# Performance work log

Hardware: AMD Instinct MI355X
Metric: run time of the kernel (lower is better)

The kernel has to match this reference:

```python
import jax, jax.numpy as jnp
import numpy as np

D_MODEL = 1024
HEAD = 16
D_K = D_MODEL // HEAD
NEG_INF = -1.0e9


def setup_inputs() -> dict:
    key = jax.random.key(0)
    ks = jax.random.split(key, 12)
    B, S = 2, 2048
    scale = 1.0 / np.sqrt(D_MODEL)
    inp = {
        "query": jax.random.normal(ks[0], (B, S, D_MODEL), jnp.float32),
        "key": jax.random.normal(ks[1], (B, S, D_MODEL), jnp.float32),
        "value": jax.random.normal(ks[2], (B, S, D_MODEL), jnp.float32),
        "mask": jax.random.randint(ks[3], (B, 1, 1, S), 0, 2, jnp.int32),
        "Wq": jax.random.normal(ks[4], (D_MODEL, D_MODEL), jnp.float32) * scale,
        "bq": jnp.zeros((D_MODEL,), jnp.float32),
        "Wk": jax.random.normal(ks[5], (D_MODEL, D_MODEL), jnp.float32) * scale,
        "bk": jnp.zeros((D_MODEL,), jnp.float32),
        "Wv": jax.random.normal(ks[6], (D_MODEL, D_MODEL), jnp.float32) * scale,
        "bv": jnp.zeros((D_MODEL,), jnp.float32),
        "Wo": jax.random.normal(ks[7], (D_MODEL, D_MODEL), jnp.float32) * scale,
        "bo": jnp.zeros((D_MODEL,), jnp.float32),
    }
    return inp


def reference(query, key, value, mask, Wq, bq, Wk, bk, Wv, bv, Wo, bo):
    B, S, _ = query.shape
    # QKV projections (torch nn.Linear: x @ W^T + b)
    q = query @ Wq.T + bq
    k = key @ Wk.T + bk
    v = value @ Wv.T + bv
    # [B, H, S, d_k]
    q = q.reshape(B, S, HEAD, D_K).transpose(0, 2, 1, 3)
    k = k.reshape(B, S, HEAD, D_K).transpose(0, 2, 1, 3)
    v = v.reshape(B, S, HEAD, D_K).transpose(0, 2, 1, 3)
    # scores [B, H, S, S]
    scores = jnp.einsum("bhqd,bhkd->bhqk", q, k) / jnp.sqrt(jnp.float32(D_K))
    scores = jnp.where(mask == 0, jnp.float32(NEG_INF), scores)
    attn = jax.nn.softmax(scores, axis=-1)  # dropout off (eval mode)
    ctx = jnp.einsum("bhqk,bhkd->bhqd", attn, v)
    ctx = ctx.transpose(0, 2, 1, 3).reshape(B, S, D_MODEL)
    return ctx @ Wo.T + bo
```

## Files before the change

kernel.cpp:

```cpp
#include <hip/hip_runtime.h>
#include <cstdint>
#include <cstddef>

typedef unsigned short u16;
typedef unsigned int   u32;
typedef __bf16 bf16x8 __attribute__((ext_vector_type(8)));
typedef float  f32x4  __attribute__((ext_vector_type(4)));

#define D_MODEL 1024
#define SEQ     2048
#define NTOK    4096
#define NHEAD   16
#define DK      64

__device__ __forceinline__ float fast_exp2(float x) {
  return __builtin_amdgcn_exp2f(x);
}

__device__ __forceinline__ u16 f2bf(float f) {
  u32 u = __builtin_bit_cast(u32, f);
  u += 0x7fffu + ((u >> 16) & 1u);
  return (u16)(u >> 16);
}

__device__ __forceinline__ void gload16(const u16* g, u16* l) {
  __builtin_amdgcn_global_load_lds(
      (__attribute__((address_space(1))) void*)(uintptr_t)g,
      (__attribute__((address_space(3))) void*)l,
      16, 0, 0);
}

__global__ __launch_bounds__(256) void mha_convert(
    const float* __restrict__ q, const float* __restrict__ k,
    const float* __restrict__ v, const float* __restrict__ wq,
    const float* __restrict__ wk, const float* __restrict__ wv,
    const float* __restrict__ wo, u16* __restrict__ xb, u16* __restrict__ wb) {
  const int total = 1 << 22;
  for (int cid = blockIdx.x * blockDim.x + threadIdx.x; cid < total;
       cid += gridDim.x * blockDim.x) {
    const float* src;
    u16* dst;
    int off;
    if (cid < (3 << 20)) {
      int which = cid >> 20;
      off = cid & ((1 << 20) - 1);
      src = which == 0 ? q : (which == 1 ? k : v);
      dst = xb + ((size_t)which << 22);
    } else {
      int cc = cid - (3 << 20);
      int which = cc >> 18;
      off = cc & ((1 << 18) - 1);
      src = which == 0 ? wq : (which == 1 ? wk : (which == 2 ? wv : wo));
      dst = wb + ((size_t)which << 20);
    }
    float4 f = ((const float4*)src)[off];
    ushort4 u;
    u.x = f2bf(f.x); u.y = f2bf(f.y); u.z = f2bf(f.z); u.w = f2bf(f.w);
    ((ushort4*)dst)[off] = u;
  }
}

__global__ __launch_bounds__(256) void gemm_qkv(
    const u16* __restrict__ A, const u16* __restrict__ Bw,
    const float* __restrict__ b0, const float* __restrict__ b1,
    const float* __restrict__ b2, u16* __restrict__ Cout) {
  __shared__ __align__(16) u16 smem[128 * 136];
  u16* sA = smem;
  u16* sB = smem + 128 * 32;

  const int t = threadIdx.x;
  const int z = blockIdx.z;
  const u16* Ap = A + ((size_t)z << 22);
  const u16* Bp = Bw + ((size_t)z << 20);
  const float* bias = (z == 0) ? b0 : ((z == 1) ? b1 : b2);
  const float scl = (z == 0) ? 0.18033688011f : 1.0f;

  const int m0 = blockIdx.y * 128, n0 = blockIdx.x * 128;
  const int lane = t & 63, wv = t >> 6;
  const int wm = (wv >> 1) * 64, wn = (wv & 1) * 64;
  const int c = lane & 15, qd = lane >> 4;

  const int arow = t >> 2, aoff = (t & 3) * 8;
  const u16* ga0 = Ap + (size_t)(m0 + arow) * D_MODEL + aoff;
  const u16* ga1 = Ap + (size_t)(m0 + arow + 64) * D_MODEL + aoff;
  const u16* gb0 = Bp + (size_t)(n0 + arow) * D_MODEL + aoff;
  const u16* gb1 = Bp + (size_t)(n0 + arow + 64) * D_MODEL + aoff;
  u16* la0 = sA + t * 8;
  u16* la1 = sA + (t + 256) * 8;
  u16* lb0 = sB + t * 8;
  u16* lb1 = sB + (t + 256) * 8;

  f32x4 acc[4][4] = {};

  for (int kb = 0; kb < D_MODEL; kb += 32) {
    gload16(ga0 + kb, la0);
    gload16(ga1 + kb, la1);
    gload16(gb0 + kb, lb0);
    gload16(gb1 + kb, lb1);
    __syncthreads();
    bf16x8 af[4], bfr[4];
#pragma unroll
    for (int i = 0; i < 4; ++i)
      af[i] = *(const bf16x8*)&sA[(wm + i * 16 + c) * 32 + qd * 8];
#pragma unroll
    for (int j = 0; j < 4; ++j)
      bfr[j] = *(const bf16x8*)&sB[(wn + j * 16 + c) * 32 + qd * 8];
#pragma unroll
    for (int i = 0; i < 4; ++i)
#pragma unroll
      for (int j = 0; j < 4; ++j)
        acc[i][j] =
            __builtin_amdgcn_mfma_f32_16x16x32_bf16(af[i], bfr[j], acc[i][j], 0, 0, 0);
    __syncthreads();
  }

  u16* sC = smem;
  if (z == 2) {
#pragma unroll
    for (int j = 0; j < 4; ++j) {
      const int col = wn + j * 16 + c;
      const float bv = bias[n0 + col];
#pragma unroll
      for (int i = 0; i < 4; ++i)
#pragma unroll
        for (int r = 0; r < 4; ++r)
          sC[col * 136 + wm + i * 16 + qd * 4 + r] = f2bf(acc[i][j][r] + bv);
    }
    __syncthreads();
    u16* VT = Cout + ((size_t)2 << 22);
    const int bb = m0 >> 11, s0 = m0 & 2047;
    const int sidx = (t & 15) * 8;
#pragma unroll
    for (int outer = 0; outer < 8; ++outer) {
      const int vrow = outer * 16 + (t >> 4);
      const int col = n0 + vrow;
      const int hh = col >> 6, dd = col & 63;
      uint4 val = *(const uint4*)&sC[vrow * 136 + sidx];
      *(uint4*)&VT[((size_t)((bb * NHEAD + hh) * DK + dd)) * SEQ + s0 + sidx] =
          val;
    }
  } else {
#pragma unroll
    for (int j = 0; j < 4; ++j) {
      const int col = wn + j * 16 + c;
      const float bv = bias[n0 + col];
#pragma unroll
      for (int i = 0; i < 4; ++i)
#pragma unroll
        for (int r = 0; r < 4; ++r)
          sC[(wm + i * 16 + qd * 4 + r) * 136 + col] =
              f2bf((acc[i][j][r] + bv) * scl);
    }
    __syncthreads();
    u16* outp = Cout + ((size_t)z << 22);
    const int cidx = (t & 15) * 8;
#pragma unroll
    for (int outer = 0; outer < 8; ++outer) {
      const int lrow = outer * 16 + (t >> 4);
      uint4 val = *(const uint4*)&sC[lrow * 136 + cidx];
      *(uint4*)&outp[(size_t)(m0 + lrow) * D_MODEL + n0 + cidx] = val;
    }
  }
}

__global__ __launch_bounds__(256) void mha_attn(
    const u16* __restrict__ QKVb, const int* __restrict__ mask,
    u16* __restrict__ Opart, float* __restrict__ ml) {
  __shared__ __align__(16) u16 sK[64 * 72];
  __shared__ __align__(16) u16 sVt[64 * 72];
  __shared__ __align__(16) u16 sP[128 * 72];
  __shared__ __align__(16) float sMadd[64];

  const int t = threadIdx.x, lane = t & 63, wq = t >> 6;
  const int c = lane & 15, qd = lane >> 4;
  const int qb = blockIdx.x, h = blockIdx.y;
  const int b = blockIdx.z & 1, ck = blockIdx.z >> 1;

  const u16* Qg = QKVb;
  const u16* Kg = QKVb + ((size_t)4 << 20);
  const u16* VTh = QKVb + ((size_t)8 << 20) +
                   ((size_t)((b * NHEAD + h) * DK)) * SEQ;
  const int rowbase = b * SEQ;
  const int colbase = h * DK;

  bf16x8 aq[2][2];
#pragma unroll
  for (int qt = 0; qt < 2; ++qt) {
    const u16* g = Qg +
                   (size_t)(rowbase + qb * 128 + wq * 32 + qt * 16 + c) * D_MODEL +
                   colbase + qd * 8;
    aq[qt][0] = *(const bf16x8*)g;
    aq[qt][1] = *(const bf16x8*)(g + 32);
  }

  float l[2] = {0.f, 0.f};
  f32x4 o[2][4] = {};
  const float MADD = -1.4426950e9f;
  const float MFIX = 16.0f;

  const int r0s = t >> 2, offs = (t & 3) * 16;
  const u16* gkb = Kg + (size_t)(rowbase + r0s) * D_MODEL + colbase + offs;
  const u16* gvb = VTh + (size_t)r0s * SEQ + offs;

  uint4 k0, k1, v0, v1;
  int mval;
  {
    const int kb = ck * 16;
    const u16* gk = gkb + (size_t)kb * 64 * D_MODEL;
    const u16* gv = gvb + kb * 64;
    k0 = *(const uint4*)gk;
    k1 = *(const uint4*)(gk + 8);
    v0 = *(const uint4*)gv;
    v1 = *(const uint4*)(gv + 8);
    mval = (t < 64) ? mask[b * SEQ + kb * 64 + t] : 1;
  }

  for (int kbi = 0; kbi < 16; ++kbi) {
    __syncthreads();
    *(uint4*)&sK[r0s * 72 + offs] = k0;
    *(uint4*)&sK[r0s * 72 + offs + 8] = k1;
    *(uint4*)&sVt[r0s * 72 + offs] = v0;
    *(uint4*)&sVt[r0s * 72 + offs + 8] = v1;
    if (t < 64) sMadd[t] = (mval == 0) ? MADD : 0.0f;
    __syncthreads();
    if (kbi < 15) {
      const int kb = ck * 16 + kbi + 1;
      const u16* gk = gkb + (size_t)kb * 64 * D_MODEL;
      const u16* gv = gvb + kb * 64;
      k0 = *(const uint4*)gk;
      k1 = *(const uint4*)(gk + 8);
      v0 = *(const uint4*)gv;
      v1 = *(const uint4*)(gv + 8);
      mval = (t < 64) ? mask[b * SEQ + kb * 64 + t] : 1;
    }

    f32x4 st[2][4];
#pragma unroll
    for (int tt = 0; tt < 4; ++tt) {
      bf16x8 ak0 = *(const bf16x8*)&sK[(tt * 16 + c) * 72 + qd * 8];
      bf16x8 ak1 = *(const bf16x8*)&sK[(tt * 16 + c) * 72 + qd * 8 + 32];
      f32x4 cin = *(const f32x4*)&sMadd[tt * 16 + qd * 4];
#pragma unroll
      for (int qt = 0; qt < 2; ++qt) {
        f32x4 a =
            __builtin_amdgcn_mfma_f32_16x16x32_bf16(ak0, aq[qt][0], cin, 0, 0, 0);
        a = __builtin_amdgcn_mfma_f32_16x16x32_bf16(ak1, aq[qt][1], a, 0, 0, 0);
        st[qt][tt] = a;
      }
    }

#pragma unroll
    for (int qt = 0; qt < 2; ++qt) {
      float sum = 0.f;
      const int prow = (wq * 32 + qt * 16 + c) * 72;
#pragma unroll
      for (int tt = 0; tt < 4; ++tt) {
        u32 pk[2];
#pragma unroll
        for (int pr = 0; pr < 2; ++pr) {
          u32 p0 = __builtin_bit_cast(u32, fast_exp2(st[qt][tt][2 * pr] - MFIX));
          u32 p1 =
              __builtin_bit_cast(u32, fast_exp2(st[qt][tt][2 * pr + 1] - MFIX));
          u32 hi1 = p1 & 0xffff0000u;
          pk[pr] = (p0 >> 16) | hi1;
          sum += __builtin_bit_cast(float, p0 & 0xffff0000u);
          sum += __builtin_bit_cast(float, hi1);
        }
        uint2 pv2 = {pk[0], pk[1]};
        *(uint2*)&sP[prow + tt * 16 + qd * 4] = pv2;
      }
      l[qt] += sum;
    }

    bf16x8 bp[2][2];
#pragma unroll
    for (int qt = 0; qt < 2; ++qt) {
      const int prow = (wq * 32 + qt * 16 + c) * 72;
      bp[qt][0] = *(const bf16x8*)&sP[prow + qd * 8];
      bp[qt][1] = *(const bf16x8*)&sP[prow + qd * 8 + 32];
    }
#pragma unroll
    for (int dt = 0; dt < 4; ++dt) {
      bf16x8 av0 = *(const bf16x8*)&sVt[(dt * 16 + c) * 72 + qd * 8];
      bf16x8 av1 = *(const bf16x8*)&sVt[(dt * 16 + c) * 72 + qd * 8 + 32];
#pragma unroll
      for (int qt = 0; qt < 2; ++qt) {
        o[qt][dt] =
            __builtin_amdgcn_mfma_f32_16x16x32_bf16(av0, bp[qt][0], o[qt][dt], 0, 0, 0);
        o[qt][dt] =
            __builtin_amdgcn_mfma_f32_16x16x32_bf16(av1, bp[qt][1], o[qt][dt], 0, 0, 0);
      }
    }
  }

  const size_t obase =
      (size_t)ck * 4194304 + ((size_t)((b * NHEAD + h) * SEQ) + qb * 128) * 64;
  const int mlbase = ((ck * 2 + b) * NHEAD + h) * SEQ + qb * 128;
#pragma unroll
  for (int qt = 0; qt < 2; ++qt) {
    float ls = l[qt];
    ls += __shfl_xor(ls, 16);
    ls += __shfl_xor(ls, 32);
    const float inv = 1.0f / ls;
    const int q = wq * 32 + qt * 16 + c;
#pragma unroll
    for (int dt = 0; dt < 4; ++dt) {
      u32 lo = (u32)f2bf(o[qt][dt][0] * inv) |
               ((u32)f2bf(o[qt][dt][1] * inv) << 16);
      u32 hi = (u32)f2bf(o[qt][dt][2] * inv) |
               ((u32)f2bf(o[qt][dt][3] * inv) << 16);
      uint2 ov = {lo, hi};
      *(uint2*)&Opart[obase + (size_t)q * 64 + dt * 16 + qd * 4] = ov;
    }
    if (qd == 0) ml[mlbase + q] = ls;
  }
}

__global__ __launch_bounds__(256) void mha_combine(
    const u16* __restrict__ Opart, const float* __restrict__ ml,
    u16* __restrict__ ctx) {
  const int tid = blockIdx.x * 256 + threadIdx.x;
  const int row = tid >> 3, d0 = (tid & 7) * 8;
  const int b = row >> 15, h = (row >> 11) & 15, q = row & 2047;
  float l1 = ml[row];
  float l2 = ml[65536 + row];
  float inv = 1.0f / (l1 + l2);
  float w1 = l1 * inv, w2 = l2 * inv;
  const size_t o1 = (size_t)row * 64 + d0;
  uint4 pa = *(const uint4*)(Opart + o1);
  uint4 pb = *(const uint4*)(Opart + 4194304 + o1);
  u32 wa[4] = {pa.x, pa.y, pa.z, pa.w};
  u32 wb[4] = {pb.x, pb.y, pb.z, pb.w};
  u32 out[4];
#pragma unroll
  for (int j = 0; j < 4; ++j) {
    float alo = __builtin_bit_cast(float, wa[j] << 16);
    float ahi = __builtin_bit_cast(float, wa[j] & 0xffff0000u);
    float blo = __builtin_bit_cast(float, wb[j] << 16);
    float bhi = __builtin_bit_cast(float, wb[j] & 0xffff0000u);
    float rlo = w1 * alo + w2 * blo;
    float rhi = w1 * ahi + w2 * bhi;
    out[j] = (u32)f2bf(rlo) | ((u32)f2bf(rhi) << 16);
  }
  uint4 ov = {out[0], out[1], out[2], out[3]};
  *(uint4*)&ctx[((size_t)(b * SEQ + q)) * D_MODEL + h * DK + d0] = ov;
}

__global__ __launch_bounds__(256) void gemm_out(
    const u16* __restrict__ A, const u16* __restrict__ Bw,
    const float* __restrict__ bias, float* __restrict__ Cout) {
  __shared__ __align__(16) u16 sA[128 * 32];
  __shared__ __align__(16) u16 sB[64 * 32];

  const int t = threadIdx.x;
  const int m0 = blockIdx.y * 128, n0 = blockIdx.x * 64;
  const int lane = t & 63, wv = t >> 6;
  const int wm = (wv >> 1) * 64, wn = (wv & 1) * 32;
  const int c = lane & 15, qd = lane >> 4;

  const int arow = t >> 2, aoff = (t & 3) * 8;
  const u16* ga0 = A + (size_t)(m0 + arow) * D_MODEL + aoff;
  const u16* ga1 = A + (size_t)(m0 + arow + 64) * D_MODEL + aoff;
  const u16* gb0 = Bw + (size_t)(n0 + arow) * D_MODEL + aoff;
  u16* la0 = sA + t * 8;
  u16* la1 = sA + (t + 256) * 8;
  u16* lb0 = sB + t * 8;

  f32x4 acc[4][2] = {};

  for (int kb = 0; kb < D_MODEL; kb += 32) {
    gload16(ga0 + kb, la0);
    gload16(ga1 + kb, la1);
    gload16(gb0 + kb, lb0);
    __syncthreads();
    bf16x8 af[4], bfr[2];
#pragma unroll
    for (int i = 0; i < 4; ++i)
      af[i] = *(const bf16x8*)&sA[(wm + i * 16 + c) * 32 + qd * 8];
#pragma unroll
    for (int j = 0; j < 2; ++j)
      bfr[j] = *(const bf16x8*)&sB[(wn + j * 16 + c) * 32 + qd * 8];
#pragma unroll
    for (int i = 0; i < 4; ++i)
#pragma unroll
      for (int j = 0; j < 2; ++j)
        acc[i][j] =
            __builtin_amdgcn_mfma_f32_16x16x32_bf16(af[i], bfr[j], acc[i][j], 0, 0, 0);
    __syncthreads();
  }

#pragma unroll
  for (int j = 0; j < 2; ++j) {
    const int col = n0 + wn + j * 16 + c;
    const float bv = bias[col];
#pragma unroll
    for (int i = 0; i < 4; ++i)
#pragma unroll
      for (int r = 0; r < 4; ++r) {
        const int row = m0 + wm + i * 16 + qd * 4 + r;
        Cout[(size_t)row * D_MODEL + col] = acc[i][j][r] + bv;
      }
  }
}

extern "C" void kernel_launch(void* const* d_in, const int* in_sizes, int n_in,
                              void* d_out, int out_size, void* d_ws,
                              size_t ws_size, hipStream_t stream) {
  const float* query = (const float*)d_in[0];
  const float* key   = (const float*)d_in[1];
  const float* value = (const float*)d_in[2];
  const int*   mask  = (const int*)d_in[3];
  const float* Wq = (const float*)d_in[4];
  const float* bq = (const float*)d_in[5];
  const float* Wk = (const float*)d_in[6];
  const float* bk = (const float*)d_in[7];
  const float* Wv = (const float*)d_in[8];
  const float* bv = (const float*)d_in[9];
  const float* Wo = (const float*)d_in[10];
  const float* bo = (const float*)d_in[11];

  u16* ws  = (u16*)d_ws;
  u16* Xb  = ws;
  u16* Wb  = ws + ((size_t)12 << 20);
  u16* QKV = ws + ((size_t)16 << 20);
  u16* CTX = ws + ((size_t)28 << 20);
  u16* Opart = ws + ((size_t)4 << 20);
  float* ml = (float*)(ws + ((size_t)12 << 20));

  mha_convert<<<dim3(4096), dim3(256), 0, stream>>>(query, key, value, Wq, Wk,
                                                    Wv, Wo, Xb, Wb);
  gemm_qkv<<<dim3(8, 32, 3), dim3(256), 0, stream>>>(Xb, Wb, bq, bk, bv, QKV);
  mha_attn<<<dim3(16, 16, 4), dim3(256), 0, stream>>>(QKV, mask, Opart, ml);
  mha_combine<<<dim3(2048), dim3(256), 0, stream>>>(Opart, ml, CTX);
  gemm_out<<<dim3(16, 32), dim3(256), 0, stream>>>(CTX, Wb + ((size_t)3 << 20),
                                                   bo, (float*)d_out);
}
```

Baseline: 249.9 us.

## Compact unmasked keys and skip masked key blocks in attention

Adds a prefix-scan kernel that builds a per-batch list of unmasked key positions and their count. A new gather kernel compacts the transposed V rows to match that list. The attention kernel then loads K rows through the index list and runs only over the compacted blocks, split between the two key chunks. This removes the QK and PV work and the memory traffic for masked keys, at the cost of two extra launches, an element-wise gather pass, and indirect K loads. A row whose keys are all masked now gets zero output, where the reference averages uniformly over all keys.

```diff
diff --git a/kernel.cpp b/kernel.cpp
--- a/kernel.cpp
+++ b/kernel.cpp
@@ -28,6 +28,45 @@
       (__attribute__((address_space(1))) void*)(uintptr_t)g,
       (__attribute__((address_space(3))) void*)l,
       16, 0, 0);
+}
+
+__global__ __launch_bounds__(256) void mask_scan(const int* __restrict__ mask,
+                                                 int* __restrict__ idx,
+                                                 int* __restrict__ cnt) {
+  const int b = blockIdx.x, t = threadIdx.x;
+  const int lane = t & 63, w = t >> 6;
+  __shared__ int sW[4];
+  __shared__ int sTot;
+  int m8[8];
+  const int base = b * SEQ + t * 8;
+  int tot = 0;
+#pragma unroll
+  for (int i = 0; i < 8; ++i) {
+    m8[i] = (mask[base + i] != 0);
+    tot += m8[i];
+  }
+  int v = tot;
+#pragma unroll
+  for (int d = 1; d < 64; d <<= 1) {
+    int u = __shfl_up(v, d);
+    if (lane >= d) v += u;
+  }
+  if (lane == 63) sW[w] = v;
+  __syncthreads();
+  if (t == 0) {
+    int run = 0;
+#pragma unroll
+    for (int i = 0; i < 4; ++i) { int tmp = sW[i]; sW[i] = run; run += tmp; }
+    sTot = run;
+  }
+  __syncthreads();
+  int pos = v - tot + sW[w];
+#pragma unroll
+  for (int i = 0; i < 8; ++i)
+    if (m8[i]) idx[b * SEQ + pos++] = t * 8 + i;
+  const int cn = sTot;
+  if (t == 0) cnt[b] = cn;
+  for (int j = cn + t; j < SEQ; j += 256) idx[b * SEQ + j] = 0;
 }
 
 __global__ __launch_bounds__(256) void mha_convert(
@@ -163,23 +202,41 @@
   }
 }
 
+__global__ __launch_bounds__(256) void vtc_gather(const u16* __restrict__ VT,
+                                                  const int* __restrict__ idx,
+                                                  const int* __restrict__ cnt,
+                                                  u16* __restrict__ VTc) {
+  const int row = blockIdx.x;
+  const int b = row >> 10;
+  const int cn = cnt[b];
+  const u16* src = VT + (size_t)row * SEQ;
+  u16* dst = VTc + (size_t)row * SEQ;
+  const int* ib = idx + b * SEQ;
+  for (int j = threadIdx.x; j < cn; j += 256) dst[j] = src[ib[j]];
+}
+
 __global__ __launch_bounds__(256) void mha_attn(
-    const u16* __restrict__ QKVb, const int* __restrict__ mask,
+    const u16* __restrict__ QKVb, const u16* __restrict__ VTc,
+    const int* __restrict__ idx, const int* __restrict__ cnt,
     u16* __restrict__ Opart, float* __restrict__ ml) {
   __shared__ __align__(16) u16 sK[64 * 72];
   __shared__ __align__(16) u16 sVt[64 * 72];
   __shared__ __align__(16) u16 sP[128 * 72];
-  __shared__ __align__(16) float sMadd[64];
 
   const int t = threadIdx.x, lane = t & 63, wq = t >> 6;
   const int c = lane & 15, qd = lane >> 4;
   const int qb = blockIdx.x, h = blockIdx.y;
   const int b = blockIdx.z & 1, ck = blockIdx.z >> 1;
 
+  const int cn = cnt[b];
+  const int nb = (cn + 63) >> 6;
+  const int half = (nb + 1) >> 1;
+  const int kstart = ck ? half : 0;
+  const int kend = ck ? nb : half;
+
   const u16* Qg = QKVb;
   const u16* Kg = QKVb + ((size_t)4 << 20);
-  const u16* VTh = QKVb + ((size_t)8 << 20) +
-                   ((size_t)((b * NHEAD + h) * DK)) * SEQ;
+  const u16* VTch = VTc + ((size_t)((b * NHEAD + h) * DK)) * SEQ;
   const int rowbase = b * SEQ;
   const int colbase = h * DK;
 
@@ -199,47 +256,53 @@
   const float MFIX = 16.0f;
 
   const int r0s = t >> 2, offs = (t & 3) * 16;
-  const u16* gkb = Kg + (size_t)(rowbase + r0s) * D_MODEL + colbase + offs;
-  const u16* gvb = VTh + (size_t)r0s * SEQ + offs;
+  const u16* gvb = VTch + (size_t)r0s * SEQ + offs;
+  const int* idxb = idx + b * SEQ + r0s;
 
   uint4 k0, k1, v0, v1;
-  int mval;
-  {
-    const int kb = ck * 16;
-    const u16* gk = gkb + (size_t)kb * 64 * D_MODEL;
-    const u16* gv = gvb + kb * 64;
+  int sNext2 = 0;
+  if (kstart < kend) {
+    const int s0i = idxb[kstart * 64];
+    const u16* gk = Kg + (size_t)(rowbase + s0i) * D_MODEL + colbase + offs;
+    const u16* gv = gvb + kstart * 64;
     k0 = *(const uint4*)gk;
     k1 = *(const uint4*)(gk + 8);
     v0 = *(const uint4*)gv;
     v1 = *(const uint4*)(gv + 8);
-    mval = (t < 64) ? mask[b * SEQ + kb * 64 + t] : 1;
-  }
-
-  for (int kbi = 0; kbi < 16; ++kbi) {
+    if (kstart + 1 < kend) sNext2 = idxb[(kstart + 1) * 64];
+  }
+
+  for (int kbi = kstart; kbi < kend; ++kbi) {
     __syncthreads();
     *(uint4*)&sK[r0s * 72 + offs] = k0;
     *(uint4*)&sK[r0s * 72 + offs + 8] = k1;
     *(uint4*)&sVt[r0s * 72 + offs] = v0;
     *(uint4*)&sVt[r0s * 72 + offs + 8] = v1;
-    if (t < 64) sMadd[t] = (mval == 0) ? MADD : 0.0f;
-    __syncthreads();
-    if (kbi < 15) {
-      const int kb = ck * 16 + kbi + 1;
-      const u16* gk = gkb + (size_t)kb * 64 * D_MODEL;
-      const u16* gv = gvb + kb * 64;
+    __syncthreads();
+    if (kbi + 1 < kend) {
+      const u16* gk = Kg + (size_t)(rowbase + sNext2) * D_MODEL + colbase + offs;
+      const u16* gv = gvb + (kbi + 1) * 64;
       k0 = *(const uint4*)gk;
       k1 = *(const uint4*)(gk + 8);
       v0 = *(const uint4*)gv;
       v1 = *(const uint4*)(gv + 8);
-      mval = (t < 64) ? mask[b * SEQ + kb * 64 + t] : 1;
-    }
-
+    }
+    if (kbi + 2 < kend) sNext2 = idxb[(kbi + 2) * 64];
+
+    const bool full = ((kbi + 1) << 6) <= cn;
     f32x4 st[2][4];
 #pragma unroll
     for (int tt = 0; tt < 4; ++tt) {
       bf16x8 ak0 = *(const bf16x8*)&sK[(tt * 16 + c) * 72 + qd * 8];
       bf16x8 ak1 = *(const bf16x8*)&sK[(tt * 16 + c) * 72 + qd * 8 + 32];
-      f32x4 cin = *(const f32x4*)&sMadd[tt * 16 + qd * 4];
+      f32x4 cin;
+      if (full) {
+        cin = f32x4{0.f, 0.f, 0.f, 0.f};
+      } else {
+        const int jb = (kbi << 6) + tt * 16 + qd * 4;
+        cin = f32x4{jb + 0 < cn ? 0.f : MADD, jb + 1 < cn ? 0.f : MADD,
+                    jb + 2 < cn ? 0.f : MADD, jb + 3 < cn ? 0.f : MADD};
+      }
 #pragma unroll
       for (int qt = 0; qt < 2; ++qt) {
         f32x4 a =
@@ -301,7 +364,7 @@
     float ls = l[qt];
     ls += __shfl_xor(ls, 16);
     ls += __shfl_xor(ls, 32);
-    const float inv = 1.0f / ls;
+    const float inv = (ls != 0.f) ? 1.0f / ls : 0.f;
     const int q = wq * 32 + qt * 16 + c;
 #pragma unroll
     for (int dt = 0; dt < 4; ++dt) {
@@ -424,13 +487,20 @@
   u16* Wb  = ws + ((size_t)12 << 20);
   u16* QKV = ws + ((size_t)16 << 20);
   u16* CTX = ws + ((size_t)28 << 20);
+  u16* VTc = ws;
   u16* Opart = ws + ((size_t)4 << 20);
   float* ml = (float*)(ws + ((size_t)12 << 20));
-
+  int* idxp = (int*)(ws + ((size_t)28 << 20));
+  int* cntp = idxp + 2 * SEQ;
+
+  mask_scan<<<dim3(2), dim3(256), 0, stream>>>(mask, idxp, cntp);
   mha_convert<<<dim3(4096), dim3(256), 0, stream>>>(query, key, value, Wq, Wk,
                                                     Wv, Wo, Xb, Wb);
   gemm_qkv<<<dim3(8, 32, 3), dim3(256), 0, stream>>>(Xb, Wb, bq, bk, bv, QKV);
-  mha_attn<<<dim3(16, 16, 4), dim3(256), 0, stream>>>(QKV, mask, Opart, ml);
+  vtc_gather<<<dim3(2048), dim3(256), 0, stream>>>(QKV + ((size_t)8 << 20), idxp,
+                                                   cntp, VTc);
+  mha_attn<<<dim3(16, 16, 4), dim3(256), 0, stream>>>(QKV, VTc, idxp, cntp,
+                                                      Opart, ml);
   mha_combine<<<dim3(2048), dim3(256), 0, stream>>>(Opart, ml, CTX);
   gemm_out<<<dim3(16, 32), dim3(256), 0, stream>>>(CTX, Wb + ((size_t)3 << 20),
                                                    bo, (float*)d_out);
```

New measurement: 237.5 us. -5.0%, faster.
